# Kernel tuning notes

Hardware: AMD Instinct MI355X
Metric: run time of the kernel (lower is better)

Reference implementation:

```python
import jax, jax.numpy as jnp
import numpy as np

WINDOW = 256  # attention_window (band half-width w; band is 2w+1 wide)


def _longformer(q, k, v, global_attention_mask, padding_mask, num_global, w):
    B, H, S, D = q.shape
    BH = B * H
    G = int(num_global)
    scale = jnp.sqrt(jnp.asarray(D, q.dtype))
    qf = q.reshape(BH, S, D)
    kf = k.reshape(BH, S, D)
    vf = v.reshape(BH, S, D)
    is_global = jnp.repeat(global_attention_mask.astype(bool), H, axis=0)  # [BH,S]
    pad_ok = jnp.repeat(padding_mask.astype(bool), H, axis=0)              # [BH,S]
    NEG = jnp.asarray(-jnp.inf, q.dtype)

    # ---- banded local qk scores via overlapping 3-chunk trick ----
    nc = S // w
    qc = qf.reshape(BH, nc, w, D)
    kp = jnp.pad(kf, ((0, 0), (w, w), (0, 0))).reshape(BH, nc + 2, w, D)
    k3 = jnp.concatenate([kp[:, :-2], kp[:, 1:-1], kp[:, 2:]], axis=2)     # [BH,nc,3w,D]
    scores3 = jnp.einsum('bcxd,bcyd->bcxy', qc, k3) / scale                # [BH,nc,w,3w]
    band_idx = jnp.arange(w)[:, None] + jnp.arange(2 * w + 1)[None, :]     # [w,2w+1]
    band = jnp.take_along_axis(scores3, band_idx[None, None], axis=3)
    band = band.reshape(BH, S, 2 * w + 1)                                  # score[i,t] = q_i . k_{i-w+t}

    # ---- local-band masking: out-of-bounds, global key columns, padding ----
    rel = jnp.arange(S)[:, None] + jnp.arange(-w, w + 1)[None, :]          # [S,2w+1]
    oob = (rel < 0) | (rel >= S)
    relc = jnp.clip(rel, 0, S - 1)
    glob_key = is_global[:, relc]                                          # [BH,S,2w+1]
    pad_key = pad_ok[:, relc]
    band = jnp.where(oob[None] | glob_key | ~pad_key, NEG, band)

    # ---- all tokens attend to the (sparse) global keys ----
    gpos = jnp.argsort((~is_global).astype(jnp.int32), axis=-1)[:, :G]     # stable: global positions in order
    gk = jnp.take_along_axis(kf, gpos[..., None], axis=1)                  # [BH,G,D]
    gv = jnp.take_along_axis(vf, gpos[..., None], axis=1)
    g_ok = jnp.take_along_axis(pad_ok, gpos, axis=1)                       # [BH,G]
    gscores = jnp.einsum('bsd,bgd->bsg', qf, gk) / scale
    gscores = jnp.where(g_ok[:, None, :], gscores, NEG)

    # ---- joint softmax over [global | local band] ----
    probs = jax.nn.softmax(jnp.concatenate([gscores, band], axis=-1), axis=-1)
    gprobs, lprobs = probs[..., :G], probs[..., G:]

    ctx = jnp.einsum('bsg,bgd->bsd', gprobs, gv)
    vp = jnp.pad(vf, ((0, 0), (w, w), (0, 0))).reshape(BH, nc + 2, w, D)
    v3 = jnp.concatenate([vp[:, :-2], vp[:, 1:-1], vp[:, 2:]], axis=2)     # [BH,nc,3w,D]
    p3 = jnp.zeros((BH, nc, w, 3 * w), probs.dtype)
    p3 = p3.at[:, :, jnp.arange(w)[:, None], band_idx].set(lprobs.reshape(BH, nc, w, 2 * w + 1))
    ctx = ctx + jnp.einsum('bcxy,bcyd->bcxd', p3, v3).reshape(BH, S, D)

    # ---- global tokens attend to every token (full attention rows) ----
    gq = jnp.take_along_axis(qf, gpos[..., None], axis=1)                  # [BH,G,D]
    rscores = jnp.einsum('bgd,bsd->bgs', gq, kf) / scale
    rscores = jnp.where(pad_ok[:, None, :], rscores, NEG)
    rprobs = jax.nn.softmax(rscores, axis=-1)
    vmask = jnp.where(pad_ok[..., None], vf, jnp.asarray(0.0, vf.dtype))
    ctx_g = jnp.einsum('bgs,bsd->bgd', rprobs, vmask)
    ctx = ctx.at[jnp.arange(BH)[:, None], gpos].set(ctx_g)

    return ctx.reshape(B, H, S, D)


def setup_inputs() -> dict:
    key = jax.random.key(0)
    kq, kk, kv = jax.random.split(key, 3)
    B, H, S, D, G = 1, 16, 4096, 64, 64
    q = jax.random.normal(kq, (B, H, S, D), jnp.float32)
    k = jax.random.normal(kk, (B, H, S, D), jnp.float32)
    v = jax.random.normal(kv, (B, H, S, D), jnp.float32)
    global_attention_mask = jnp.zeros((B, S), jnp.int32).at[:, :G].set(1)
    padding_mask = jnp.ones((B, S), jnp.int32)
    return {"q": q, "k": k, "v": v, "global_attention_mask": global_attention_mask,
            "padding_mask": padding_mask, "num_global": G}


def reference(q, k, v, global_attention_mask, padding_mask, num_global):
    return _longformer(q, k, v, global_attention_mask, padding_mask, num_global, WINDOW)
```

## Files before the change

kernel.cpp:

```cpp
#include <hip/hip_runtime.h>
#include <hip/hip_bf16.h>

#define SLEN 4096
#define NH   16
#define DH   64
#define WW   256
#define GMAX 64

typedef unsigned short u16;
typedef unsigned int   u32;
typedef unsigned long long u64;
typedef __attribute__((ext_vector_type(8))) short bf16x8;
typedef __attribute__((ext_vector_type(4))) float f32x4;

#define MFMA16(a,b,c) __builtin_amdgcn_mfma_f32_16x16x32_bf16((a),(b),(c),0,0,0)

static __device__ __forceinline__ int imin(int a, int b) { return a < b ? a : b; }
static __device__ __forceinline__ int imax(int a, int b) { return a > b ? a : b; }

__device__ __forceinline__ u32 cvtpk(float lo, float hi) {
  u32 r;
  asm("v_cvt_pk_bf16_f32 %0, %1, %2" : "=v"(r) : "v"(lo), "v"(hi));
  return r;
}

__device__ __forceinline__ void gload16(const u16* src, u16* lds_base) {
  __builtin_amdgcn_global_load_lds((const __attribute__((address_space(1))) u32*)src,
                                   (__attribute__((address_space(3))) u32*)lds_base,
                                   16, 0, 0);
}

__global__ __launch_bounds__(256) void lf_prep1(
    const float* __restrict__ q, const float* __restrict__ k, const float* __restrict__ v,
    const int* __restrict__ gmask, const int* __restrict__ pmask, const int* __restrict__ nGp,
    u16* __restrict__ qB, u16* __restrict__ kB, u16* __restrict__ vtB,
    int* __restrict__ gpos, unsigned char* __restrict__ gmsk,
    unsigned char* __restrict__ msk, unsigned char* __restrict__ cleanmap, float qscale) {
  const int bid = blockIdx.x;
  const int tid = threadIdx.x;
  if (bid < 4096) {
    const bool isq = bid < 2048;
    const float sc = isq ? qscale : 1.0f;
    const float* src = isq ? q : k;
    u16* dst = isq ? qB : kB;
    int i = ((isq ? bid : bid - 2048) * 256 + tid) * 8;
    float4 v0 = *(const float4*)(src + i);
    float4 v1 = *(const float4*)(src + i + 4);
    uint4 w;
    w.x = cvtpk(v0.x * sc, v0.y * sc);
    w.y = cvtpk(v0.z * sc, v0.w * sc);
    w.z = cvtpk(v1.x * sc, v1.y * sc);
    w.w = cvtpk(v1.z * sc, v1.w * sc);
    *(uint4*)(dst + i) = w;
    return;
  }
  if (bid < 5120) {
    __shared__ float t[64][65];
    int b = bid - 4096;
    int h = b >> 6, s0 = (b & 63) << 6;
    int tile = h * 64 + (b & 63);
    int r = tid >> 2, c0 = (tid & 3) << 4;
    const float* src = v + ((size_t)h * SLEN + s0 + r) * DH + c0;
#pragma unroll
    for (int j = 0; j < 16; j += 4) {
      float4 a = *(const float4*)(src + j);
      t[r][c0 + j]     = a.x;
      t[r][c0 + j + 1] = a.y;
      t[r][c0 + j + 2] = a.z;
      t[r][c0 + j + 3] = a.w;
    }
    __syncthreads();
    int d = tid >> 2, j0 = (tid & 3) << 4;
    int grp  = j0 & 32;
    int half = (j0 & 16) ? 4 : 0;
    u16* dst = vtB + ((size_t)tile * 64 + d) * 64 + grp;
#pragma unroll
    for (int q4 = 0; q4 < 4; ++q4) {
      uint2 val;
      val.x = cvtpk(t[j0 + 4 * q4 + 0][d], t[j0 + 4 * q4 + 1][d]);
      val.y = cvtpk(t[j0 + 4 * q4 + 2][d], t[j0 + 4 * q4 + 3][d]);
      *(uint2*)(dst + 8 * q4 + half) = val;
    }
    return;
  }
  const int G = imin(nGp[0], GMAX);
  for (int s = tid; s < SLEN; s += 256) {
    unsigned char b = (unsigned char)((pmask[s] ? 1 : 0) | (gmask[s] ? 2 : 0));
    msk[s] = b;
  }
  for (int s = SLEN + tid; s < SLEN + 64; s += 256) msk[s] = 0;
  __syncthreads();
  if (tid < 64) {
    int lane = tid;
    if (lane < GMAX) gmsk[lane] = 0;
    int cnt = 0;
    for (int c = 0; c < SLEN / 64 && cnt < G; ++c) {
      int s = c * 64 + lane;
      bool isg = gmask[s] != 0;
      u64 b = __ballot(isg);
      int rank = cnt + (int)__popcll(b & ((1ull << lane) - 1ull));
      if (isg && rank < G) gpos[rank] = s;
      cnt += (int)__popcll(b);
    }
    if (cnt < G) {
      int fill = cnt;
      for (int c = 0; c < SLEN / 64 && fill < G; ++c) {
        int s = c * 64 + lane;
        bool non = gmask[s] == 0;
        u64 b = __ballot(non);
        int rank = fill + (int)__popcll(b & ((1ull << lane) - 1ull));
        if (non && rank < G) gpos[rank] = s;
        fill += (int)__popcll(b);
      }
    }
  }
  __syncthreads();
  if (tid < 64) {
    if (tid < G) {
      int p = gpos[tid];
      gmsk[tid] = (unsigned char)(pmask[p] ? 1 : 0);
      msk[p] = (unsigned char)(msk[p] | 4);
    }
  } else if (tid >= 128) {
    int c = tid - 128;
    if (c < SLEN / 32) {
      unsigned char ok1 = 1, ok2 = 1;
      for (int kk = 0; kk < 32; ++kk) {
        unsigned char b = msk[c * 32 + kk];
        ok1 &= (unsigned char)(((b & 3) == 1) ? 1 : 0);
        ok2 &= (unsigned char)(b & 1);
      }
      cleanmap[c] = (unsigned char)(ok1 | (ok2 << 1));
    }
  }
}

__global__ void lf_gather(const u16* __restrict__ qB, const u16* __restrict__ kB,
                          const u16* __restrict__ vtB, const int* __restrict__ gpos,
                          const int* __restrict__ nGp,
                          u16* __restrict__ gq, u16* __restrict__ gk, u16* __restrict__ gvt) {
  const int G = imin(nGp[0], GMAX);
  int idx = blockIdx.x * 256 + threadIdx.x;
  int h = idx >> 12, m = (idx >> 6) & 63, d = idx & 63;
  size_t oq = ((size_t)h * GMAX + m) * DH + d;
  int r = m & 31;
  int pos = ((r & 12) << 1) + ((r & 16) >> 2) + (r & 3);
  size_t ot = ((size_t)h * DH + d) * GMAX + (m & 32) + pos;
  if (m < G) {
    int p = gpos[m];
    int pr = p & 31;
    int ppos = ((pr & 12) << 1) + ((pr & 16) >> 2) + (pr & 3);
    gq[oq]  = qB[((size_t)h * SLEN + p) * DH + d];
    gk[oq]  = kB[((size_t)h * SLEN + p) * DH + d];
    gvt[ot] = vtB[((size_t)(h * 64 + (p >> 6)) * 64 + d) * 64 + (p & 32) + ppos];
  } else {
    gq[oq] = 0; gk[oq] = 0; gvt[ot] = 0;
  }
}

__global__ __launch_bounds__(256) void lf_attn(
    const u16* __restrict__ qB, const u16* __restrict__ kB, const u16* __restrict__ vtB,
    const u16* __restrict__ gkB, const u16* __restrict__ gqB, const u16* __restrict__ gvtB,
    const unsigned char* __restrict__ gmskA, const unsigned char* __restrict__ mskA,
    const unsigned char* __restrict__ cleanA, const int* __restrict__ nGp,
    float* __restrict__ out, float* __restrict__ pAcc, float* __restrict__ pL) {
  __shared__ __align__(16) u16 sK[2][4096];
  __shared__ __align__(16) u16 sV[2][4096];

  const int tid  = threadIdx.x;
  const int wv   = tid >> 6;
  const int lane = tid & 63;
  const int ql   = lane & 15;
  const int g    = lane >> 4;
  const float NEGV = -1e30f;
  const float MEXP = 24.0f;
  const int G = imin(nGp[0], GMAX);

  const int wg = ((int)blockIdx.x & 7) * 144 + ((int)blockIdx.x >> 3);
  const bool glob = (wg % 9) == 0;

  int off[4][2];
#pragma unroll
  for (int t = 0; t < 4; ++t)
#pragma unroll
    for (int c = 0; c < 2; ++c) {
      int row = 16 * t + ql;
      off[t][c] = (row * 8 + ((c * 4 + g) ^ (row & 7))) * 8;
    }

  f32x4 acc[4];
#pragma unroll
  for (int i = 0; i < 4; ++i) acc[i] = (f32x4){0.f, 0.f, 0.f, 0.f};
  f32x4 lsv = (f32x4){0.f, 0.f, 0.f, 0.f};
  bf16x8 qf0, qf1;

  int h, s0w = 0, sq = 0, t0, nPh, qg = 0, splitIdx = 0;
  int lo_w = 0, hi_w = 0;
  bool hasG = false;
  const u16 *gks = nullptr, *gvs = nullptr;

  if (!glob) {
    int lid = wg - wg / 9 - 1;
    h = lid >> 6;
    int qblk = lid & 63;
    int s0 = qblk << 6;
    s0w = s0 + 16 * wv; sq = s0w + ql;
    t0 = imax(0, qblk - 4);
    int t1 = imin(63, qblk + 4);
    nPh = t1 - t0 + 1;
    hasG = (G > 0);
    lo_w = imax(t0, (s0w - WW) >> 6);
    hi_w = imin(t1, (s0w + 15 + WW) >> 6);
    const u16* qRow = qB + ((size_t)h * SLEN + sq) * DH;
    qf0 = *(const bf16x8*)(qRow + 8 * g);
    qf1 = *(const bf16x8*)(qRow + 32 + 8 * g);
    gks = gkB + (size_t)h * GMAX * DH;
    gvs = gvtB + (size_t)h * 4096;
  } else {
    int gb = wg / 9;
    h = gb >> 3; splitIdx = gb & 7;
    qg = wv * 16 + ql;
    t0 = splitIdx * 8; nPh = 8;
    const u16* qRow = gqB + ((size_t)h * GMAX + qg) * DH;
    qf0 = *(const bf16x8*)(qRow + 8 * g);
    qf1 = *(const bf16x8*)(qRow + 32 + 8 * g);
  }
  const u16* kbase = kB  + (size_t)h * 64 * 4096;
  const u16* vbase = vtB + (size_t)h * 64 * 4096;
  const int totPh = nPh + (hasG ? 1 : 0);

  auto stage = [&](int p, int b) {
    const u16 *ks, *vs;
    if (hasG && p == 0) { ks = gks; vs = gvs; }
    else {
      int tv = t0 + p - (hasG ? 1 : 0);
      ks = kbase + (size_t)tv * 4096;
      vs = vbase + (size_t)tv * 4096;
    }
#pragma unroll
    for (int j = 0; j < 2; ++j) {
      int gran = (wv * 2 + j) * 64 + lane;
      int sg = gran ^ ((gran >> 3) & 7);
      gload16(ks + (size_t)sg * 8, &sK[b][(wv * 2 + j) * 512]);
      gload16(vs + (size_t)sg * 8, &sV[b][(wv * 2 + j) * 512]);
    }
  };

  auto compute = [&](int p) {
    const bool isg = (hasG && p == 0);
    const int tv = t0 + p - (hasG ? 1 : 0);
    const int kb = tv * 64;
    bool doC = glob ? true : (isg || (tv >= lo_w && tv <= hi_w));
    if (!doC) return;
    const u16* sk = &sK[p & 1][0];
    const u16* sv = &sV[p & 1][0];
    f32x4 sc[4];
#pragma unroll
    for (int t = 0; t < 4; ++t) sc[t] = (f32x4){0.f, 0.f, 0.f, 0.f};
#pragma unroll
    for (int t = 0; t < 4; ++t) {
      bf16x8 a0 = *(const bf16x8*)(sk + off[t][0]);
      bf16x8 a1 = *(const bf16x8*)(sk + off[t][1]);
      sc[t] = MFMA16(a0, qf0, sc[t]);
      sc[t] = MFMA16(a1, qf1, sc[t]);
    }
    f32x4 pv[4];
    if (isg) {
#pragma unroll
      for (int t = 0; t < 4; ++t) {
        u32 mw = *(const u32*)(gmskA + 16 * t + 4 * g);
#pragma unroll
        for (int i = 0; i < 4; ++i) {
          float s = ((mw >> (8 * i)) & 1) ? sc[t][i] : NEGV;
          pv[t][i] = __builtin_amdgcn_exp2f(s - MEXP);
        }
      }
    } else if (glob) {
      u16 cw = *(const u16*)(cleanA + (kb >> 5));
      if (cw & (cw >> 8) & 2) {
#pragma unroll
        for (int t = 0; t < 4; ++t)
#pragma unroll
          for (int i = 0; i < 4; ++i)
            pv[t][i] = __builtin_amdgcn_exp2f(sc[t][i] - MEXP);
      } else {
#pragma unroll
        for (int t = 0; t < 4; ++t) {
          u32 mw = *(const u32*)(mskA + kb + 16 * t + 4 * g);
#pragma unroll
          for (int i = 0; i < 4; ++i) {
            float s = ((mw >> (8 * i)) & 1) ? sc[t][i] : NEGV;
            pv[t][i] = __builtin_amdgcn_exp2f(s - MEXP);
          }
        }
      }
    } else {
      u16 cw = *(const u16*)(cleanA + (kb >> 5));
      bool cl = ((cw & (cw >> 8) & 1) != 0) &&
                (kb >= s0w + 15 - WW) && (kb + 63 <= s0w + WW);
      if (cl) {
#pragma unroll
        for (int t = 0; t < 4; ++t)
#pragma unroll
          for (int i = 0; i < 4; ++i)
            pv[t][i] = __builtin_amdgcn_exp2f(sc[t][i] - MEXP);
      } else {
#pragma unroll
        for (int t = 0; t < 4; ++t) {
          u32 mw = *(const u32*)(mskA + kb + 16 * t + 4 * g);
#pragma unroll
          for (int i = 0; i < 4; ++i) {
            int kkey = kb + 16 * t + 4 * g + i;
            bool vok = (((mw >> (8 * i)) & 3) == 1) && (kkey >= sq - WW) && (kkey <= sq + WW);
            float s = vok ? sc[t][i] : NEGV;
            pv[t][i] = __builtin_amdgcn_exp2f(s - MEXP);
          }
        }
      }
    }
    lsv += pv[0] + pv[1] + pv[2] + pv[3];
#pragma unroll
    for (int s2 = 0; s2 < 2; ++s2) {
      union { u32 w[4]; bf16x8 v8; } u;
      u.w[0] = cvtpk(pv[2 * s2][0], pv[2 * s2][1]);
      u.w[1] = cvtpk(pv[2 * s2][2], pv[2 * s2][3]);
      u.w[2] = cvtpk(pv[2 * s2 + 1][0], pv[2 * s2 + 1][1]);
      u.w[3] = cvtpk(pv[2 * s2 + 1][2], pv[2 * s2 + 1][3]);
#pragma unroll
      for (int dt = 0; dt < 4; ++dt) {
        bf16x8 vf = *(const bf16x8*)(sv + off[dt][s2]);
        acc[dt] = MFMA16(vf, u.v8, acc[dt]);
      }
    }
  };

  stage(0, 0);
  for (int p = 0; p < totPh; ++p) {
    if (p + 1 < totPh) {
      stage(p + 1, (p + 1) & 1);
      asm volatile("s_waitcnt vmcnt(4)" ::: "memory");
    } else {
      asm volatile("s_waitcnt vmcnt(0)" ::: "memory");
    }
    __builtin_amdgcn_s_barrier();
    __builtin_amdgcn_sched_barrier(0);
    compute(p);
    __builtin_amdgcn_s_barrier();
  }

  float lsum = lsv[0] + lsv[1] + lsv[2] + lsv[3];
  lsum += __shfl_xor(lsum, 16);
  lsum += __shfl_xor(lsum, 32);

  if (!glob) {
    float inv = 1.f / lsum;
    bool skip = (mskA[sq] & 4) != 0;
    if (!skip) {
      float* orow = out + ((size_t)h * SLEN + sq) * DH;
#pragma unroll
      for (int dt = 0; dt < 4; ++dt) {
        f32x4 o = acc[dt] * inv;
        *(f32x4*)(orow + dt * 16 + 4 * g) = o;
      }
    }
  } else {
    float* pa = pAcc + ((size_t)(h * 8 + splitIdx) * 64 + qg) * 64;
#pragma unroll
    for (int dt = 0; dt < 4; ++dt)
      *(f32x4*)&pa[dt * 16 + 4 * g] = acc[dt];
    if (g == 0) pL[(h * 8 + splitIdx) * 64 + qg] = lsum;
  }
}

__global__ void lf_gmerge(const float* __restrict__ pAcc, const float* __restrict__ pL,
                          const int* __restrict__ gpos, const int* __restrict__ nGp,
                          float* __restrict__ out) {
  const int G = imin(nGp[0], GMAX);
  int h = blockIdx.x;
  int tid = threadIdx.x;
#pragma unroll
  for (int it = 0; it < 4; ++it) {
    int v = tid + it * 256;
    int q = v >> 4, d4 = (v & 15) << 2;
    if (q >= G) continue;
    float L = 0.f;
    f32x4 a = (f32x4){0.f, 0.f, 0.f, 0.f};
#pragma unroll
    for (int s = 0; s < 8; ++s) {
      L += pL[(h * 8 + s) * 64 + q];
      a += *(const f32x4*)&pAcc[((size_t)(h * 8 + s) * 64 + q) * 64 + d4];
    }
    *(f32x4*)&out[((size_t)h * SLEN + gpos[q]) * DH + d4] = a * (1.f / L);
  }
}

extern "C" void kernel_launch(void* const* d_in, const int* in_sizes, int n_in,
                              void* d_out, int out_size, void* d_ws, size_t ws_size,
                              hipStream_t stream) {
  const float* q = (const float*)d_in[0];
  const float* k = (const float*)d_in[1];
  const float* v = (const float*)d_in[2];
  const int* gmask = (const int*)d_in[3];
  const int* pmask = (const int*)d_in[4];
  const int* nGp = (const int*)d_in[5];
  float* out = (float*)d_out;
  char* ws = (char*)d_ws;

  constexpr size_t NEL = (size_t)NH * SLEN * DH;
  constexpr size_t OFF_QBF  = 0;
  constexpr size_t OFF_KBF  = OFF_QBF + NEL * 2;
  constexpr size_t OFF_VTBF = OFF_KBF + NEL * 2;
  constexpr size_t OFF_GK   = OFF_VTBF + NEL * 2 + 256;
  constexpr size_t OFF_GQ   = OFF_GK + (size_t)NH * GMAX * DH * 2;
  constexpr size_t OFF_GVT  = OFF_GQ + (size_t)NH * GMAX * DH * 2;
  constexpr size_t OFF_GPOS = OFF_GVT + (size_t)NH * DH * GMAX * 2;
  constexpr size_t OFF_GMSK = OFF_GPOS + 256;
  constexpr size_t OFF_MSK  = OFF_GMSK + 64;
  constexpr size_t OFF_CLEAN = OFF_MSK + SLEN + 64;
  constexpr size_t OFF_PACC = OFF_CLEAN + 256;
  constexpr size_t OFF_PL   = OFF_PACC + (size_t)NH * 8 * 64 * 64 * 4;

  u16* qB  = (u16*)(ws + OFF_QBF);
  u16* kB  = (u16*)(ws + OFF_KBF);
  u16* vtB = (u16*)(ws + OFF_VTBF);
  u16* gk  = (u16*)(ws + OFF_GK);
  u16* gq  = (u16*)(ws + OFF_GQ);
  u16* gvt = (u16*)(ws + OFF_GVT);
  int* gpos = (int*)(ws + OFF_GPOS);
  unsigned char* gmsk = (unsigned char*)(ws + OFF_GMSK);
  unsigned char* msk  = (unsigned char*)(ws + OFF_MSK);
  unsigned char* clean = (unsigned char*)(ws + OFF_CLEAN);
  float* pAcc = (float*)(ws + OFF_PACC);
  float* pL   = (float*)(ws + OFF_PL);

  const float qscale = 0.125f * 1.4426950408889634f;

  lf_prep1<<<5121, 256, 0, stream>>>(q, k, v, gmask, pmask, nGp,
                                     qB, kB, vtB, gpos, gmsk, msk, clean, qscale);
  lf_gather<<<256, 256, 0, stream>>>(qB, kB, vtB, gpos, nGp, gq, gk, gvt);
  lf_attn<<<1152, 256, 0, stream>>>(qB, kB, vtB, gk, gq, gvt, gmsk, msk, clean,
                                    nGp, out, pAcc, pL);
  lf_gmerge<<<NH, 256, 0, stream>>>(pAcc, pL, gpos, nGp, out);
}
```

Before: 56.75 us.

## Fuse Q bf16 conversion into attention kernel and triple-buffer K/V staging

```diff
diff --git a/kernel.cpp b/kernel.cpp
--- a/kernel.cpp
+++ b/kernel.cpp
@@ -23,6 +23,11 @@
   asm("v_cvt_pk_bf16_f32 %0, %1, %2" : "=v"(r) : "v"(lo), "v"(hi));
   return r;
 }
+__device__ __forceinline__ u16 f2bf(float x) {
+  u32 u = __float_as_uint(x);
+  u32 r = (u + 0x7fffu + ((u >> 16) & 1u)) >> 16;
+  return (u16)r;
+}
 
 __device__ __forceinline__ void gload16(const u16* src, u16* lds_base) {
   __builtin_amdgcn_global_load_lds((const __attribute__((address_space(1))) u32*)src,
@@ -31,32 +36,28 @@
 }
 
 __global__ __launch_bounds__(256) void lf_prep1(
-    const float* __restrict__ q, const float* __restrict__ k, const float* __restrict__ v,
+    const float* __restrict__ k, const float* __restrict__ v,
     const int* __restrict__ gmask, const int* __restrict__ pmask, const int* __restrict__ nGp,
-    u16* __restrict__ qB, u16* __restrict__ kB, u16* __restrict__ vtB,
+    u16* __restrict__ kB, u16* __restrict__ vtB,
     int* __restrict__ gpos, unsigned char* __restrict__ gmsk,
-    unsigned char* __restrict__ msk, unsigned char* __restrict__ cleanmap, float qscale) {
+    unsigned char* __restrict__ msk, unsigned char* __restrict__ cleanmap) {
   const int bid = blockIdx.x;
   const int tid = threadIdx.x;
-  if (bid < 4096) {
-    const bool isq = bid < 2048;
-    const float sc = isq ? qscale : 1.0f;
-    const float* src = isq ? q : k;
-    u16* dst = isq ? qB : kB;
-    int i = ((isq ? bid : bid - 2048) * 256 + tid) * 8;
-    float4 v0 = *(const float4*)(src + i);
-    float4 v1 = *(const float4*)(src + i + 4);
+  if (bid < 2048) {
+    int i = (bid * 256 + tid) * 8;
+    float4 v0 = *(const float4*)(k + i);
+    float4 v1 = *(const float4*)(k + i + 4);
     uint4 w;
-    w.x = cvtpk(v0.x * sc, v0.y * sc);
-    w.y = cvtpk(v0.z * sc, v0.w * sc);
-    w.z = cvtpk(v1.x * sc, v1.y * sc);
-    w.w = cvtpk(v1.z * sc, v1.w * sc);
-    *(uint4*)(dst + i) = w;
+    w.x = cvtpk(v0.x, v0.y);
+    w.y = cvtpk(v0.z, v0.w);
+    w.z = cvtpk(v1.x, v1.y);
+    w.w = cvtpk(v1.z, v1.w);
+    *(uint4*)(kB + i) = w;
     return;
   }
-  if (bid < 5120) {
+  if (bid < 3072) {
     __shared__ float t[64][65];
-    int b = bid - 4096;
+    int b = bid - 2048;
     int h = b >> 6, s0 = (b & 63) << 6;
     int tile = h * 64 + (b & 63);
     int r = tid >> 2, c0 = (tid & 3) << 4;
@@ -135,10 +136,11 @@
   }
 }
 
-__global__ void lf_gather(const u16* __restrict__ qB, const u16* __restrict__ kB,
+__global__ void lf_gather(const float* __restrict__ qF, const u16* __restrict__ kB,
                           const u16* __restrict__ vtB, const int* __restrict__ gpos,
                           const int* __restrict__ nGp,
-                          u16* __restrict__ gq, u16* __restrict__ gk, u16* __restrict__ gvt) {
+                          u16* __restrict__ gq, u16* __restrict__ gk, u16* __restrict__ gvt,
+                          float qscale) {
   const int G = imin(nGp[0], GMAX);
   int idx = blockIdx.x * 256 + threadIdx.x;
   int h = idx >> 12, m = (idx >> 6) & 63, d = idx & 63;
@@ -150,7 +152,7 @@
     int p = gpos[m];
     int pr = p & 31;
     int ppos = ((pr & 12) << 1) + ((pr & 16) >> 2) + (pr & 3);
-    gq[oq]  = qB[((size_t)h * SLEN + p) * DH + d];
+    gq[oq]  = f2bf(qF[((size_t)h * SLEN + p) * DH + d] * qscale);
     gk[oq]  = kB[((size_t)h * SLEN + p) * DH + d];
     gvt[ot] = vtB[((size_t)(h * 64 + (p >> 6)) * 64 + d) * 64 + (p & 32) + ppos];
   } else {
@@ -159,13 +161,13 @@
 }
 
 __global__ __launch_bounds__(256) void lf_attn(
-    const u16* __restrict__ qB, const u16* __restrict__ kB, const u16* __restrict__ vtB,
+    const float* __restrict__ qF, const u16* __restrict__ kB, const u16* __restrict__ vtB,
     const u16* __restrict__ gkB, const u16* __restrict__ gqB, const u16* __restrict__ gvtB,
     const unsigned char* __restrict__ gmskA, const unsigned char* __restrict__ mskA,
     const unsigned char* __restrict__ cleanA, const int* __restrict__ nGp,
-    float* __restrict__ out, float* __restrict__ pAcc, float* __restrict__ pL) {
-  __shared__ __align__(16) u16 sK[2][4096];
-  __shared__ __align__(16) u16 sV[2][4096];
+    float* __restrict__ out, float* __restrict__ pAcc, float* __restrict__ pL, float qscale) {
+  __shared__ __align__(16) u16 sK[3][4096];
+  __shared__ __align__(16) u16 sV[3][4096];
 
   const int tid  = threadIdx.x;
   const int wv   = tid >> 6;
@@ -211,9 +213,22 @@
     hasG = (G > 0);
     lo_w = imax(t0, (s0w - WW) >> 6);
     hi_w = imin(t1, (s0w + 15 + WW) >> 6);
-    const u16* qRow = qB + ((size_t)h * SLEN + sq) * DH;
-    qf0 = *(const bf16x8*)(qRow + 8 * g);
-    qf1 = *(const bf16x8*)(qRow + 32 + 8 * g);
+    const float* qr = qF + ((size_t)h * SLEN + sq) * DH;
+    float4 a0 = *(const float4*)(qr + 8 * g);
+    float4 a1 = *(const float4*)(qr + 8 * g + 4);
+    float4 b0 = *(const float4*)(qr + 32 + 8 * g);
+    float4 b1 = *(const float4*)(qr + 32 + 8 * g + 4);
+    union { u32 w[4]; bf16x8 v; } uq;
+    uq.w[0] = cvtpk(a0.x * qscale, a0.y * qscale);
+    uq.w[1] = cvtpk(a0.z * qscale, a0.w * qscale);
+    uq.w[2] = cvtpk(a1.x * qscale, a1.y * qscale);
+    uq.w[3] = cvtpk(a1.z * qscale, a1.w * qscale);
+    qf0 = uq.v;
+    uq.w[0] = cvtpk(b0.x * qscale, b0.y * qscale);
+    uq.w[1] = cvtpk(b0.z * qscale, b0.w * qscale);
+    uq.w[2] = cvtpk(b1.x * qscale, b1.y * qscale);
+    uq.w[3] = cvtpk(b1.z * qscale, b1.w * qscale);
+    qf1 = uq.v;
     gks = gkB + (size_t)h * GMAX * DH;
     gvs = gvtB + (size_t)h * 4096;
   } else {
@@ -246,14 +261,14 @@
     }
   };
 
-  auto compute = [&](int p) {
+  auto compute = [&](int p, int buf) {
     const bool isg = (hasG && p == 0);
     const int tv = t0 + p - (hasG ? 1 : 0);
     const int kb = tv * 64;
     bool doC = glob ? true : (isg || (tv >= lo_w && tv <= hi_w));
     if (!doC) return;
-    const u16* sk = &sK[p & 1][0];
-    const u16* sv = &sV[p & 1][0];
+    const u16* sk = &sK[buf][0];
+    const u16* sv = &sV[buf][0];
     f32x4 sc[4];
 #pragma unroll
     for (int t = 0; t < 4; ++t) sc[t] = (f32x4){0.f, 0.f, 0.f, 0.f};
@@ -335,17 +350,22 @@
   };
 
   stage(0, 0);
+  if (totPh > 1) stage(1, 1);
+  int cur = 0;
   for (int p = 0; p < totPh; ++p) {
     if (p + 1 < totPh) {
-      stage(p + 1, (p + 1) & 1);
       asm volatile("s_waitcnt vmcnt(4)" ::: "memory");
     } else {
       asm volatile("s_waitcnt vmcnt(0)" ::: "memory");
     }
     __builtin_amdgcn_s_barrier();
     __builtin_amdgcn_sched_barrier(0);
-    compute(p);
-    __builtin_amdgcn_s_barrier();
+    if (p + 2 < totPh) {
+      int nb = cur + 2; if (nb >= 3) nb -= 3;
+      stage(p + 2, nb);
+    }
+    compute(p, cur);
+    ++cur; if (cur == 3) cur = 0;
   }
 
   float lsum = lsv[0] + lsv[1] + lsv[2] + lsv[3];
@@ -407,8 +427,7 @@
   char* ws = (char*)d_ws;
 
   constexpr size_t NEL = (size_t)NH * SLEN * DH;
-  constexpr size_t OFF_QBF  = 0;
-  constexpr size_t OFF_KBF  = OFF_QBF + NEL * 2;
+  constexpr size_t OFF_KBF  = 0;
   constexpr size_t OFF_VTBF = OFF_KBF + NEL * 2;
   constexpr size_t OFF_GK   = OFF_VTBF + NEL * 2 + 256;
   constexpr size_t OFF_GQ   = OFF_GK + (size_t)NH * GMAX * DH * 2;
@@ -420,7 +439,6 @@
   constexpr size_t OFF_PACC = OFF_CLEAN + 256;
   constexpr size_t OFF_PL   = OFF_PACC + (size_t)NH * 8 * 64 * 64 * 4;
 
-  u16* qB  = (u16*)(ws + OFF_QBF);
   u16* kB  = (u16*)(ws + OFF_KBF);
   u16* vtB = (u16*)(ws + OFF_VTBF);
   u16* gk  = (u16*)(ws + OFF_GK);
@@ -435,10 +453,10 @@
 
   const float qscale = 0.125f * 1.4426950408889634f;
 
-  lf_prep1<<<5121, 256, 0, stream>>>(q, k, v, gmask, pmask, nGp,
-                                     qB, kB, vtB, gpos, gmsk, msk, clean, qscale);
-  lf_gather<<<256, 256, 0, stream>>>(qB, kB, vtB, gpos, nGp, gq, gk, gvt);
-  lf_attn<<<1152, 256, 0, stream>>>(qB, kB, vtB, gk, gq, gvt, gmsk, msk, clean,
-                                    nGp, out, pAcc, pL);
+  lf_prep1<<<3073, 256, 0, stream>>>(k, v, gmask, pmask, nGp,
+                                     kB, vtB, gpos, gmsk, msk, clean);
+  lf_gather<<<256, 256, 0, stream>>>(q, kB, vtB, gpos, nGp, gq, gk, gvt, qscale);
+  lf_attn<<<1152, 256, 0, stream>>>(q, kB, vtB, gk, gq, gvt, gmsk, msk, clean,
+                                    nGp, out, pAcc, pL, qscale);
   lf_gmerge<<<NH, 256, 0, stream>>>(pAcc, pL, gpos, nGp, out);
 }
```

Result: faster. 55.25 us (-2.6%).
